# Kernel optimization log

Measured on AMD Instinct MI355X. Metric: run time of the kernel, lower is better.

## Reference

```python
import jax, jax.numpy as jnp
import numpy as np

D_MODEL = 1024
NUM_HEADS = 16
HEAD_DIM = D_MODEL // NUM_HEADS
D_FF = 4096
THETA = 10000.0
MAX_SEQ_LEN = 2048
EPS = 1e-5


def _init_linear(key, out_f, in_f):
    std = np.sqrt(2.0 / (out_f + in_f))
    w = jax.random.truncated_normal(key, -3.0, 3.0, (out_f, in_f), dtype=jnp.float32) * std
    return w


def setup_inputs() -> dict:
    key = jax.random.key(0)
    ks = jax.random.split(key, 9)
    x = jax.random.normal(ks[0], (4, 2048, D_MODEL), dtype=jnp.float32)
    return {
        "x": x,
        "wq": _init_linear(ks[1], D_MODEL, D_MODEL),
        "wk": _init_linear(ks[2], D_MODEL, D_MODEL),
        "wv": _init_linear(ks[3], D_MODEL, D_MODEL),
        "wo": _init_linear(ks[4], D_MODEL, D_MODEL),
        "ln1_w": jnp.ones((D_MODEL,), jnp.float32),
        "ln2_w": jnp.ones((D_MODEL,), jnp.float32),
        "up_w": _init_linear(ks[5], D_FF, D_MODEL),
        "gate_w": _init_linear(ks[6], D_FF, D_MODEL),
        "down_w": _init_linear(ks[7], D_MODEL, D_FF),
    }


def _rmsnorm(x, w):
    xf = x.astype(jnp.float32)
    inv_rms = jax.lax.rsqrt(jnp.mean(xf * xf, axis=-1, keepdims=True) + EPS)
    return (xf * inv_rms * w).astype(x.dtype)


def _rope_tables(seq_len):
    inv_freq = 1.0 / THETA ** (jnp.arange(0, HEAD_DIM, 2, dtype=jnp.float32) / HEAD_DIM)
    t = jnp.arange(seq_len, dtype=jnp.float32)
    freqs = jnp.outer(t, inv_freq)  # [s, hd/2]
    return jnp.cos(freqs), jnp.sin(freqs)


def _apply_rope(x, cos, sin):
    # x: [b, h, s, hd]; cos/sin: [s, hd/2] -> broadcast over b,h
    xe = x[..., 0::2]
    xo = x[..., 1::2]
    oe = xe * cos - xo * sin
    oo = xo * cos + xe * sin
    return jnp.stack((oe, oo), axis=-1).reshape(x.shape)


def reference(x, wq, wk, wv, wo, ln1_w, ln2_w, up_w, gate_w, down_w):
    b, s, d = x.shape
    h, hd = NUM_HEADS, HEAD_DIM

    # --- attention sublayer (pre-norm) ---
    xn = _rmsnorm(x, ln1_w)
    q = (xn @ wq.T).reshape(b, s, h, hd).transpose(0, 2, 1, 3)
    k = (xn @ wk.T).reshape(b, s, h, hd).transpose(0, 2, 1, 3)
    v = (xn @ wv.T).reshape(b, s, h, hd).transpose(0, 2, 1, 3)

    cos, sin = _rope_tables(s)
    q = _apply_rope(q, cos, sin)
    k = _apply_rope(k, cos, sin)

    scale = 1.0 / jnp.sqrt(jnp.float32(hd))
    logits = jnp.einsum("bhqd,bhkd->bhqk", q, k)
    causal = jnp.tril(jnp.ones((s, s), dtype=bool))
    logits = jnp.where(causal, logits, -jnp.inf)
    attn = jax.nn.softmax(logits * scale, axis=-1)
    ao = jnp.einsum("bhqk,bhkd->bhqd", attn, v)
    ao = ao.transpose(0, 2, 1, 3).reshape(b, s, d) @ wo.T
    x = x + ao

    # --- SwiGLU FFN sublayer (pre-norm) ---
    xn = _rmsnorm(x, ln2_w)
    up = xn @ up_w.T
    gate = xn @ gate_w.T
    ff = (up * jax.nn.sigmoid(up) * gate) @ down_w.T
    return x + ff
```

## Files before the change

### kernel.cpp

```cpp
#include <hip/hip_runtime.h>
#include <stdint.h>

#define SEQ   2048
#define NTOK  8192

typedef unsigned short u16;
typedef __bf16 bf16x8 __attribute__((ext_vector_type(8)));
typedef float  f32x4  __attribute__((ext_vector_type(4)));
typedef float  f32x16 __attribute__((ext_vector_type(16)));

__device__ __forceinline__ float b2f(u16 b) {
    union { unsigned u; float f; } v; v.u = ((unsigned)b) << 16; return v.f;
}
__device__ __forceinline__ u16 f2b(float f) {
    union { float f; unsigned u; } v; v.f = f;
    unsigned r = (v.u + 0x7fffu + ((v.u >> 16) & 1u)) >> 16;
    return (u16)r;
}
__device__ __forceinline__ u16 f2b_trunc(float f) {
    union { float f; unsigned u; } v; v.f = f;
    return (u16)(v.u >> 16);
}

__device__ __forceinline__ void gl_lds16(const void* g, void* l) {
    __builtin_amdgcn_global_load_lds(
        (const __attribute__((address_space(1))) void*)g,
        (__attribute__((address_space(3))) void*)l,
        16, 0, 0);
}

__global__ __launch_bounds__(256)
void cvt_all(const float* __restrict__ wq, const float* __restrict__ wk,
             const float* __restrict__ wv, const float* __restrict__ wo,
             const float* __restrict__ wup, const float* __restrict__ wgt,
             const float* __restrict__ wdn,
             u16* __restrict__ dq, u16* __restrict__ dk, u16* __restrict__ dv,
             u16* __restrict__ dw, u16* __restrict__ dmu, u16* __restrict__ dd)
{
    const int bid = blockIdx.x;
    const float* s; u16* d; int osrc, odst;
    if (bid < 4096) {
        const int which = bid >> 10;
        osrc = odst = (bid & 1023) * 256 + threadIdx.x;
        s = which == 0 ? wq : which == 1 ? wk : which == 2 ? wv : wo;
        d = which == 0 ? dq : which == 1 ? dk : which == 2 ? dv : dw;
    } else {
        const int which = (bid - 4096) >> 12;
        const int o = ((bid - 4096) & 4095) * 256 + threadIdx.x;
        osrc = o;
        if (which == 2) { s = wdn; d = dd; odst = o; }
        else {
            s = which == 0 ? wup : wgt;
            d = dmu;
            const int row = o >> 8;
            const int rowp = ((row >> 4) << 5) + (row & 15) + (which == 0 ? 16 : 0);
            odst = rowp * 256 + (o & 255);
        }
    }
    float4 v = ((const float4*)s)[osrc];
    ushort4 ov;
    ov.x = f2b(v.x); ov.y = f2b(v.y); ov.z = f2b(v.z); ov.w = f2b(v.w);
    ((ushort4*)d)[odst] = ov;
}

template<int EPI>
__global__ __launch_bounds__(256)
void gemm_bt(const u16* __restrict__ A, const u16* __restrict__ B,
             void* __restrict__ C, const void* __restrict__ E,
             int M, int N, int K, int ldc, int coff)
{
    __shared__ __align__(16) u16 As[128 * 64];
    __shared__ __align__(16) u16 Bs[128 * 64];

    const int tid  = threadIdx.x;
    const int lane = tid & 63;
    const int wid  = tid >> 6;
    const int m0 = blockIdx.y * 128;
    const int n0 = blockIdx.x * 128;
    const int wm = (wid >> 1) * 64;
    const int wn = (wid & 1) * 64;
    const int l31 = lane & 31, kg = lane >> 5;

    f32x16 acc[2][2];
#pragma unroll
    for (int i = 0; i < 2; i++)
#pragma unroll
        for (int j = 0; j < 2; j++)
#pragma unroll
            for (int r = 0; r < 16; r++) acc[i][j][r] = 0.f;

    const u16* Ag[4]; const u16* Bg[4]; u16* Al[4]; u16* Bl[4];
#pragma unroll
    for (int j = 0; j < 4; j++) {
        const int q = j * 256 + tid;
        const int r = q >> 3, s = q & 7, c = s ^ (r & 7);
        Ag[j] = A + (size_t)(m0 + r) * K + c * 8;
        Bg[j] = B + (size_t)(n0 + r) * K + c * 8;
        Al[j] = As + q * 8;
        Bl[j] = Bs + q * 8;
    }

    int arow[2], brow[2];
#pragma unroll
    for (int i = 0; i < 2; i++) { arow[i] = wm + i * 32 + l31; }
#pragma unroll
    for (int j = 0; j < 2; j++) { brow[j] = wn + j * 32 + l31; }

    for (int kt = 0; kt < K; kt += 64) {
        __syncthreads();
#pragma unroll
        for (int j = 0; j < 4; j++) {
            gl_lds16(Ag[j] + kt, Al[j]);
            gl_lds16(Bg[j] + kt, Bl[j]);
        }
        __syncthreads();

#pragma unroll
        for (int s = 0; s < 4; s++) {
            const int ch = s * 2 + kg;
            bf16x8 af[2], bf[2];
#pragma unroll
            for (int i = 0; i < 2; i++)
                af[i] = *(const bf16x8*)(
                    &As[arow[i] * 64 + ((ch ^ (arow[i] & 7)) * 8)]);
#pragma unroll
            for (int j = 0; j < 2; j++)
                bf[j] = *(const bf16x8*)(
                    &Bs[brow[j] * 64 + ((ch ^ (brow[j] & 7)) * 8)]);
#pragma unroll
            for (int i = 0; i < 2; i++)
#pragma unroll
                for (int j = 0; j < 2; j++)
                    acc[i][j] = __builtin_amdgcn_mfma_f32_32x32x16_bf16(
                        af[i], bf[j], acc[i][j], 0, 0, 0);
        }
    }

#pragma unroll
    for (int i = 0; i < 2; i++) {
#pragma unroll
        for (int r = 0; r < 16; r++) {
            const int row = m0 + wm + i * 32 + (r & 3) + 8 * (r >> 2) + 4 * kg;
#pragma unroll
            for (int j = 0; j < 2; j++) {
                const int col = n0 + wn + j * 32 + l31;
                const size_t idx = (size_t)row * ldc + coff + col;
                const float v = acc[i][j][r];
                if (EPI == 0) {
                    ((u16*)C)[idx] = f2b(v);
                } else {
                    ((float*)C)[idx] = v + ((const float*)E)[idx];
                }
            }
        }
    }
}

#define MIDBAR \
    __builtin_amdgcn_s_barrier(); \
    asm volatile("s_waitcnt lgkmcnt(0)" ::: "memory"); \
    __builtin_amdgcn_sched_barrier(0);

#define PBAR \
    __builtin_amdgcn_s_barrier(); \
    asm volatile("" ::: "memory"); \
    __builtin_amdgcn_sched_barrier(0);

#define VMBARN(n) \
    asm volatile("s_waitcnt vmcnt(" #n ")" ::: "memory"); \
    __builtin_amdgcn_s_barrier(); \
    asm volatile("" ::: "memory"); \
    __builtin_amdgcn_sched_barrier(0);

#define LDA(bufi, mh) { \
    const u16* _ab = Ab##bufi + (mh) * 4096; \
    _Pragma("unroll") \
    for (int _m = 0; _m < 4; ++_m) { \
        Aq[_m][0] = *(const bf16x8*)(_ab + _m * 1024 + axor0); \
        Aq[_m][1] = *(const bf16x8*)(_ab + _m * 1024 + axor1); \
    } }

#define LDB(bufi, nh) { \
    const u16* _bb = Bb##bufi + (nh) * 2048; \
    _Pragma("unroll") \
    for (int _n = 0; _n < 2; ++_n) { \
        Bq[nh][_n][0] = *(const bf16x8*)(_bb + _n * 1024 + axor0); \
        Bq[nh][_n][1] = *(const bf16x8*)(_bb + _n * 1024 + axor1); \
    } }

#define MM(mh, nh) \
    __builtin_amdgcn_s_setprio(1); \
    { _Pragma("unroll") \
      for (int _m = 0; _m < 4; ++_m) { \
        _Pragma("unroll") \
        for (int _n = 0; _n < 2; ++_n) { \
            acc[(mh)*4+_m][(nh)*2+_n] = __builtin_amdgcn_mfma_f32_16x16x32_bf16( \
                Aq[_m][0], Bq[nh][_n][0], acc[(mh)*4+_m][(nh)*2+_n], 0, 0, 0); \
            acc[(mh)*4+_m][(nh)*2+_n] = __builtin_amdgcn_mfma_f32_16x16x32_bf16( \
                Aq[_m][1], Bq[nh][_n][1], acc[(mh)*4+_m][(nh)*2+_n], 0, 0, 0); \
        } } } \
    __builtin_amdgcn_s_setprio(0);

#define STAGE_A(tile, half) { \
    const u16* _s = pA0 + (size_t)(half) * 131072 + (size_t)(tile) * 64; \
    u16* _d = lA0 + ((tile) & 1) * 16384 + (half) * 8192; \
    gl_lds16(_s, _d); \
    gl_lds16(_s + 65536, _d + 4096); }

#define STAGE_B(tile, half) { \
    const u16* _s = pB0 + (size_t)(half) * 131072 + (size_t)(tile) * 64; \
    u16* _d = lB0 + ((tile) & 1) * 16384 + (half) * 8192; \
    gl_lds16(_s, _d); \
    gl_lds16(_s + 65536, _d + 4096); }

__global__ __launch_bounds__(512, 2)
void gemm8_mlp(const u16* __restrict__ A, const u16* __restrict__ Bc,
               u16* __restrict__ H)
{
    __shared__ __align__(16) u16 As[32768];
    __shared__ __align__(16) u16 Bs[32768];

    const int tid = threadIdx.x, lane = tid & 63, wid = tid >> 6;
    const int wr = wid >> 2, wc = wid & 3;
    const int r15 = lane & 15, ks = lane >> 4;
    const int m0 = blockIdx.y * 256, n0 = blockIdx.x * 256;

    const int axor0 = ((ks) ^ (r15 & 7)) * 8;
    const int axor1 = ((4 + ks) ^ (r15 & 7)) * 8;
    const u16* Ab0 = As + wr * 8192 + r15 * 64;
    const u16* Ab1 = As + 16384 + wr * 8192 + r15 * 64;
    const u16* Bb0 = Bs + (wc >> 1) * 8192 + (wc & 1) * 4096 + r15 * 64;
    const u16* Bb1 = Bs + 16384 + (wc >> 1) * 8192 + (wc & 1) * 4096 + r15 * 64;

    const int r0 = tid >> 3, c0 = (tid & 7) ^ (r0 & 7);
    const u16* pA0 = A  + (size_t)(m0 + r0) * 1024 + c0 * 8;
    const u16* pB0 = Bc + (size_t)(n0 + r0) * 1024 + c0 * 8;
    u16* lA0 = As + tid * 8;
    u16* lB0 = Bs + tid * 8;

    f32x4 acc[8][4];
#pragma unroll
    for (int m = 0; m < 8; ++m)
#pragma unroll
        for (int n = 0; n < 4; ++n)
            acc[m][n] = (f32x4){0.f, 0.f, 0.f, 0.f};

    bf16x8 Aq[4][2], Bq[2][2][2];

    STAGE_A(0, 0); STAGE_A(0, 1);
    STAGE_B(0, 0); STAGE_B(0, 1);
    STAGE_B(1, 0); STAGE_B(1, 1);
    asm volatile("s_waitcnt vmcnt(4)" ::: "memory");
    __builtin_amdgcn_s_barrier();
    asm volatile("" ::: "memory");
    __builtin_amdgcn_sched_barrier(0);

    for (int i = 0; i < 8; ++i) {
        const int t1 = 2 * i + 1;
        const int t2 = 2 * i + 2;
        const int t3 = 2 * i + 3;
        const bool st = (i < 7);

        LDA(0, 0); LDB(0, 0);
        STAGE_A(t1, 0);
        MIDBAR; MM(0, 0); PBAR;
        LDB(0, 1);
        STAGE_A(t1, 1);
        MIDBAR; MM(0, 1); PBAR;
        LDA(0, 1);
        if (st) STAGE_B(t2, 0);
        MIDBAR; MM(1, 1); PBAR;
        if (st) STAGE_B(t2, 1);
        MIDBAR; MM(1, 0);
        if (i == 7) { VMBARN(0); } else { VMBARN(4); }

        LDA(1, 0); LDB(1, 0);
        if (st) STAGE_A(t2, 0);
        MIDBAR; MM(0, 0); PBAR;
        LDB(1, 1);
        if (st) STAGE_A(t2, 1);
        MIDBAR; MM(0, 1); PBAR;
        LDA(1, 1);
        if (st) STAGE_B(t3, 0);
        MIDBAR; MM(1, 1); PBAR;
        if (st) STAGE_B(t3, 1);
        MIDBAR; MM(1, 0);
        VMBARN(4);
    }

    const int orow0 = m0 + wr * 128;
    const int ocol0 = (n0 >> 1) + wc * 32;
#pragma unroll
    for (int m = 0; m < 8; ++m) {
#pragma unroll
        for (int p = 0; p < 2; ++p) {
#pragma unroll
            for (int r = 0; r < 4; ++r) {
                const int row = orow0 + m * 16 + ks * 4 + r;
                const int col = ocol0 + p * 16 + r15;
                const float g = acc[m][2 * p][r];
                const float u = acc[m][2 * p + 1][r];
                H[(size_t)row * 4096 + col] = f2b(u / (1.f + __expf(-u)) * g);
            }
        }
    }
}

__global__ __launch_bounds__(256)
void rmsnorm_k(const float* __restrict__ xin, const float* __restrict__ w,
               u16* __restrict__ o)
{
    const int t = blockIdx.x;
    const int tid = threadIdx.x;
    float4 xv = ((const float4*)xin)[(size_t)t * 256 + tid];
    float ss = xv.x * xv.x + xv.y * xv.y + xv.z * xv.z + xv.w * xv.w;
#pragma unroll
    for (int off = 32; off > 0; off >>= 1) ss += __shfl_down(ss, off);
    __shared__ float red[4];
    const int lane = tid & 63, wv_ = tid >> 6;
    if (lane == 0) red[wv_] = ss;
    __syncthreads();
    const float tot = red[0] + red[1] + red[2] + red[3];
    const float inv = rsqrtf(tot * (1.f / 1024.f) + 1e-5f);
    float4 ww = ((const float4*)w)[tid];
    ushort4 ov;
    ov.x = f2b(xv.x * inv * ww.x);
    ov.y = f2b(xv.y * inv * ww.y);
    ov.z = f2b(xv.z * inv * ww.z);
    ov.w = f2b(xv.w * inv * ww.w);
    ((ushort4*)o)[(size_t)t * 256 + tid] = ov;
}

#define QSCALE 0.18033688011112042f

__global__ void rope_tab(float* __restrict__ cs, float* __restrict__ sn)
{
    const int s = blockIdx.x;
    const int i = threadIdx.x;
    const double inv = exp(-((double)(2 * i) / 64.0) * log(10000.0));
    const double ang = (double)s * inv;
    cs[s * 32 + i] = (float)cos(ang);
    sn[s * 32 + i] = (float)sin(ang);
}

__global__ __launch_bounds__(256)
void rope_apply(u16* __restrict__ qkv, const float* __restrict__ cs,
                const float* __restrict__ sn)
{
    const int t = blockIdx.x;
    const int s = t & (SEQ - 1);
    u16* row = qkv + (size_t)t * 3072;
    __shared__ float c_s[32], s_s[32];
    if (threadIdx.x < 32) {
        c_s[threadIdx.x] = cs[s * 32 + threadIdx.x];
        s_s[threadIdx.x] = sn[s * 32 + threadIdx.x];
    }
    __syncthreads();
#pragma unroll
    for (int rr = 0; rr < 2; rr++) {
        const int item = rr * 256 + threadIdx.x;
        const int hh = item >> 5, i = item & 31;
        const int f = hh * 64 + 2 * i;
        const float c = c_s[i], sv = s_s[i];
        float xe = b2f(row[f]), xo = b2f(row[f + 1]);
        row[f]     = f2b((xe * c - xo * sv) * QSCALE);
        row[f + 1] = f2b((xo * c + xe * sv) * QSCALE);
        xe = b2f(row[1024 + f]); xo = b2f(row[1024 + f + 1]);
        row[1024 + f]     = f2b(xe * c - xo * sv);
        row[1024 + f + 1] = f2b(xo * c + xe * sv);
    }
}

__global__ __launch_bounds__(256)
void vtrans(const u16* __restrict__ qkv, u16* __restrict__ vt)
{
    __shared__ u16 Ld[64 * 264];
    const int bh = blockIdx.x, st = blockIdx.y;
    const int b = bh >> 4, h = bh & 15;
    const int tid = threadIdx.x;
    const u16* src = qkv + ((size_t)(b * SEQ + st * 256 + tid)) * 3072 + 2048 + h * 64;
    uint4 v[8];
#pragma unroll
    for (int c = 0; c < 8; c++) v[c] = *(const uint4*)(src + c * 8);
#pragma unroll
    for (int c = 0; c < 8; c++) {
        const u16* pv = (const u16*)&v[c];
#pragma unroll
        for (int j = 0; j < 8; j++)
            Ld[(c * 8 + j) * 264 + tid] = pv[j];
    }
    __syncthreads();
    u16* dst = vt + (size_t)bh * (64 * SEQ) + st * 256;
#pragma unroll
    for (int cc = 0; cc < 8; cc++) {
        const int c = cc * 256 + tid;
        const int d = c >> 5, t8 = (c & 31) * 8;
        *(uint4*)(dst + (size_t)d * SEQ + t8) = *(const uint4*)(&Ld[d * 264 + t8]);
    }
}

__global__ __launch_bounds__(512)
void attn(const u16* __restrict__ qkv, const u16* __restrict__ vt,
          u16* __restrict__ ao)
{
    __shared__ __align__(16) u16 Ks[128 * 72];
    __shared__ __align__(16) u16 Vt[64 * 136];
    __shared__ __align__(16) u16 Ps[8][16 * 136];

    const int bh = blockIdx.x;
    const int qy = blockIdx.y;
    const int b = bh >> 4, h = bh & 15;
    const int tid = threadIdx.x, lane = tid & 63, wid = tid >> 6;
    const int am = lane & 15, grp = lane >> 4;
    const size_t tok0 = (size_t)b * SEQ;
    const u16* qbase = qkv + tok0 * 3072 + h * 64;
    const u16* kbase = qbase + 1024;
    const u16* vtg = vt + (size_t)bh * (64 * SEQ);

    union { uint4 u; bf16x8 b; } onesu;
    onesu.u = (uint4){0x3f803f80u, 0x3f803f80u, 0x3f803f80u, 0x3f803f80u};
    const bf16x8 ones = onesu.b;

    const int srow = tid >> 3, sc8 = (tid & 7) * 8;

#pragma unroll
    for (int tile = 0; tile < 2; tile++) {
        const int yt = tile == 0 ? qy : 15 - qy;
        const int qrow0 = yt * 128 + wid * 16;

        bf16x8 qf[2];
        {
            const u16* qp = qbase + (size_t)(qrow0 + am) * 3072 + grp * 8;
            qf[0] = *(const bf16x8*)(qp);
            qf[1] = *(const bf16x8*)(qp + 32);
        }

        f32x4 O[4], Ol;
#pragma unroll
        for (int j = 0; j < 4; j++) O[j] = (f32x4){0.f, 0.f, 0.f, 0.f};
        Ol = (f32x4){0.f, 0.f, 0.f, 0.f};

        const int ktend = yt * 128;
        for (int kt = 0; kt <= ktend; kt += 128) {
            __syncthreads();
            *(uint4*)(&Ks[srow * 72 + sc8]) =
                *(const uint4*)(kbase + (size_t)(kt + srow) * 3072 + sc8);
            *(uint4*)(&Ks[(srow + 64) * 72 + sc8]) =
                *(const uint4*)(kbase + (size_t)(kt + srow + 64) * 3072 + sc8);
            *(uint4*)(&Vt[srow * 136 + sc8]) =
                *(const uint4*)(vtg + (size_t)srow * SEQ + kt + sc8);
            *(uint4*)(&Vt[srow * 136 + 64 + sc8]) =
                *(const uint4*)(vtg + (size_t)srow * SEQ + kt + 64 + sc8);
            __syncthreads();

            const bool diag = (kt == ktend);
            u16* pw = &Ps[wid][0];

#pragma unroll
            for (int kh = 0; kh < 2; kh++) {
                f32x4 st[4];
#pragma unroll
                for (int kk = 0; kk < 4; kk++) {
                    const u16* kb = &Ks[(kh * 64 + kk * 16 + am) * 72 + grp * 8];
                    bf16x8 k0 = *(const bf16x8*)(kb);
                    bf16x8 k1 = *(const bf16x8*)(kb + 32);
                    f32x4 s = (f32x4){0.f, 0.f, 0.f, 0.f};
                    s = __builtin_amdgcn_mfma_f32_16x16x32_bf16(k0, qf[0], s, 0, 0, 0);
                    s = __builtin_amdgcn_mfma_f32_16x16x32_bf16(k1, qf[1], s, 0, 0, 0);
                    st[kk] = s;
                }
                if (diag) {
                    const int qg = qrow0 + am;
#pragma unroll
                    for (int kk = 0; kk < 4; kk++) {
                        const int kb2 = kt + kh * 64 + kk * 16 + grp * 4;
#pragma unroll
                        for (int r = 0; r < 4; r++) {
                            if (kb2 + r > qg) st[kk][r] = -1e30f;
                        }
                    }
                }
#pragma unroll
                for (int kk = 0; kk < 4; kk++)
#pragma unroll
                    for (int r = 0; r < 4; r++)
                        st[kk][r] = exp2f(st[kk][r]);

#pragma unroll
                for (int kk = 0; kk < 4; kk++) {
                    ushort4 pk;
                    pk.x = f2b_trunc(st[kk][0]);
                    pk.y = f2b_trunc(st[kk][1]);
                    pk.z = f2b_trunc(st[kk][2]);
                    pk.w = f2b_trunc(st[kk][3]);
                    *(ushort4*)(&pw[am * 136 + kh * 64 + kk * 16 + grp * 4]) = pk;
                }
            }
            asm volatile("s_waitcnt lgkmcnt(0)" ::: "memory");

#pragma unroll
            for (int hh = 0; hh < 4; hh++) {
                bf16x8 pf = *(const bf16x8*)(&pw[am * 136 + hh * 32 + grp * 8]);
                Ol = __builtin_amdgcn_mfma_f32_16x16x32_bf16(pf, ones, Ol, 0, 0, 0);
#pragma unroll
                for (int jt = 0; jt < 4; jt++) {
                    bf16x8 vf = *(const bf16x8*)(
                        &Vt[(jt * 16 + am) * 136 + hh * 32 + grp * 8]);
                    O[jt] = __builtin_amdgcn_mfma_f32_16x16x32_bf16(
                        pf, vf, O[jt], 0, 0, 0);
                }
            }
        }

        u16* aorow = ao + (tok0 + qrow0) * 1024 + h * 64;
#pragma unroll
        for (int r = 0; r < 4; r++) {
            const int q = grp * 4 + r;
            const float invl = 1.f / Ol[r];
#pragma unroll
            for (int jt = 0; jt < 4; jt++)
                aorow[(size_t)q * 1024 + jt * 16 + am] = f2b(O[jt][r] * invl);
        }
    }
}

extern "C" void kernel_launch(void* const* d_in, const int* in_sizes, int n_in,
                              void* d_out, int out_size, void* d_ws, size_t ws_size,
                              hipStream_t stream)
{
    (void)in_sizes; (void)n_in; (void)out_size; (void)ws_size;
    const float* x     = (const float*)d_in[0];
    const float* wq    = (const float*)d_in[1];
    const float* wk    = (const float*)d_in[2];
    const float* wv    = (const float*)d_in[3];
    const float* wo    = (const float*)d_in[4];
    const float* ln1   = (const float*)d_in[5];
    const float* ln2   = (const float*)d_in[6];
    const float* wup   = (const float*)d_in[7];
    const float* wgate = (const float*)d_in[8];
    const float* wdown = (const float*)d_in[9];
    float* out = (float*)d_out;
    char* ws = (char*)d_ws;
    const size_t MB = 1024 * 1024;

    u16*   xn   = (u16*)(ws);
    u16*   ao   = (u16*)(ws);
    u16*   qkv  = (u16*)(ws + 16 * MB);
    u16*   hbuf = (u16*)(ws + 16 * MB);
    u16*   vtb  = (u16*)(ws + 64 * MB);
    float* x1   = (float*)(ws + 80 * MB);
    u16*   bwq  = (u16*)(ws + 112 * MB);
    u16*   bwk  = (u16*)(ws + 114 * MB);
    u16*   bwv  = (u16*)(ws + 116 * MB);
    u16*   bwo  = (u16*)(ws + 118 * MB);
    u16*   bwmu = (u16*)(ws + 120 * MB);
    u16*   bwdn = (u16*)(ws + 136 * MB);
    float* cst  = (float*)(ws + 144 * MB);
    float* snt  = (float*)(ws + 144 * MB + 262144);

    cvt_all<<<16384, 256, 0, stream>>>(wq, wk, wv, wo, wup, wgate, wdown,
                                       bwq, bwk, bwv, bwo, bwmu, bwdn);

    rope_tab<<<SEQ, 32, 0, stream>>>(cst, snt);
    rmsnorm_k<<<NTOK, 256, 0, stream>>>(x, ln1, xn);
    gemm_bt<0><<<dim3(24, 64), 256, 0, stream>>>(xn, bwq, qkv, nullptr, NTOK, 3072, 1024, 3072, 0);
    rope_apply<<<NTOK, 256, 0, stream>>>(qkv, cst, snt);
    vtrans<<<dim3(64, 8), 256, 0, stream>>>(qkv, vtb);
    attn<<<dim3(64, 8), 512, 0, stream>>>(qkv, vtb, ao);
    gemm_bt<1><<<dim3(8, 64), 256, 0, stream>>>(ao, bwo, x1, x, NTOK, 1024, 1024, 1024, 0);
    rmsnorm_k<<<NTOK, 256, 0, stream>>>(x1, ln2, xn);
    gemm8_mlp<<<dim3(32, 32), 512, 0, stream>>>(xn, bwmu, hbuf);
    gemm_bt<1><<<dim3(8, 64), 256, 0, stream>>>(hbuf, bwdn, out, x1, NTOK, 1024, 4096, 1024, 0);
}
```

Baseline: 564.5 us.

## Make MLP GEMM blocks loop over four M tiles with continuous prefetch

The fused up/gate GEMM now launches a quarter as many blocks, and each block walks four consecutive 256-row M tiles. The global-to-LDS staging pipeline runs unbroken across tile boundaries, and each tile's SwiGLU epilogue is written before the accumulators are reset. This removes per-block prologue and pipeline-fill costs and may improve L2 reuse of the B tile. In exchange the grid drops from 1024 to 256 blocks, which is about one wave on 256 CUs, so tail and occupancy behaviour changes.

```diff
diff --git a/kernel.cpp b/kernel.cpp
--- a/kernel.cpp
+++ b/kernel.cpp
@@ -201,15 +201,16 @@
         } } } \
     __builtin_amdgcn_s_setprio(0);
 
-#define STAGE_A(tile, half) { \
-    const u16* _s = pA0 + (size_t)(half) * 131072 + (size_t)(tile) * 64; \
-    u16* _d = lA0 + ((tile) & 1) * 16384 + (half) * 8192; \
+#define STAGE_A(T, half) { \
+    const u16* _s = pA0 + (size_t)((T) >> 4) * 262144 \
+                        + (size_t)((T) & 15) * 64 + (size_t)(half) * 131072; \
+    u16* _d = lA0 + ((T) & 1) * 16384 + (half) * 8192; \
     gl_lds16(_s, _d); \
     gl_lds16(_s + 65536, _d + 4096); }
 
-#define STAGE_B(tile, half) { \
-    const u16* _s = pB0 + (size_t)(half) * 131072 + (size_t)(tile) * 64; \
-    u16* _d = lB0 + ((tile) & 1) * 16384 + (half) * 8192; \
+#define STAGE_B(T, half) { \
+    const u16* _s = pB0 + (size_t)((T) & 15) * 64 + (size_t)(half) * 131072; \
+    u16* _d = lB0 + ((T) & 1) * 16384 + (half) * 8192; \
     gl_lds16(_s, _d); \
     gl_lds16(_s + 65536, _d + 4096); }
 
@@ -223,7 +224,7 @@
     const int tid = threadIdx.x, lane = tid & 63, wid = tid >> 6;
     const int wr = wid >> 2, wc = wid & 3;
     const int r15 = lane & 15, ks = lane >> 4;
-    const int m0 = blockIdx.y * 256, n0 = blockIdx.x * 256;
+    const int m0 = blockIdx.y * 1024, n0 = blockIdx.x * 256;
 
     const int axor0 = ((ks) ^ (r15 & 7)) * 8;
     const int axor1 = ((4 + ks) ^ (r15 & 7)) * 8;
@@ -255,54 +256,63 @@
     asm volatile("" ::: "memory");
     __builtin_amdgcn_sched_barrier(0);
 
-    for (int i = 0; i < 8; ++i) {
-        const int t1 = 2 * i + 1;
-        const int t2 = 2 * i + 2;
-        const int t3 = 2 * i + 3;
-        const bool st = (i < 7);
-
-        LDA(0, 0); LDB(0, 0);
-        STAGE_A(t1, 0);
-        MIDBAR; MM(0, 0); PBAR;
-        LDB(0, 1);
-        STAGE_A(t1, 1);
-        MIDBAR; MM(0, 1); PBAR;
-        LDA(0, 1);
-        if (st) STAGE_B(t2, 0);
-        MIDBAR; MM(1, 1); PBAR;
-        if (st) STAGE_B(t2, 1);
-        MIDBAR; MM(1, 0);
-        if (i == 7) { VMBARN(0); } else { VMBARN(4); }
-
-        LDA(1, 0); LDB(1, 0);
-        if (st) STAGE_A(t2, 0);
-        MIDBAR; MM(0, 0); PBAR;
-        LDB(1, 1);
-        if (st) STAGE_A(t2, 1);
-        MIDBAR; MM(0, 1); PBAR;
-        LDA(1, 1);
-        if (st) STAGE_B(t3, 0);
-        MIDBAR; MM(1, 1); PBAR;
-        if (st) STAGE_B(t3, 1);
-        MIDBAR; MM(1, 0);
-        VMBARN(4);
-    }
-
-    const int orow0 = m0 + wr * 128;
-    const int ocol0 = (n0 >> 1) + wc * 32;
-#pragma unroll
-    for (int m = 0; m < 8; ++m) {
-#pragma unroll
-        for (int p = 0; p < 2; ++p) {
-#pragma unroll
-            for (int r = 0; r < 4; ++r) {
-                const int row = orow0 + m * 16 + ks * 4 + r;
-                const int col = ocol0 + p * 16 + r15;
-                const float g = acc[m][2 * p][r];
-                const float u = acc[m][2 * p + 1][r];
-                H[(size_t)row * 4096 + col] = f2b(u / (1.f + __expf(-u)) * g);
+    for (int hm = 0; hm < 4; ++hm) {
+        const int base = hm * 16;
+        for (int i = 0; i < 8; ++i) {
+            const int t1 = base + 2 * i + 1;
+            const int t2 = base + 2 * i + 2;
+            const int t3 = base + 2 * i + 3;
+            const bool s2 = (t2 < 64);
+            const bool s3 = (t3 < 64);
+
+            LDA(0, 0); LDB(0, 0);
+            STAGE_A(t1, 0);
+            MIDBAR; MM(0, 0); PBAR;
+            LDB(0, 1);
+            STAGE_A(t1, 1);
+            MIDBAR; MM(0, 1); PBAR;
+            LDA(0, 1);
+            if (s2) STAGE_B(t2, 0);
+            MIDBAR; MM(1, 1); PBAR;
+            if (s2) STAGE_B(t2, 1);
+            MIDBAR; MM(1, 0);
+            if (s2) { VMBARN(4); } else { VMBARN(0); }
+
+            LDA(1, 0); LDB(1, 0);
+            if (s2) STAGE_A(t2, 0);
+            MIDBAR; MM(0, 0); PBAR;
+            LDB(1, 1);
+            if (s2) STAGE_A(t2, 1);
+            MIDBAR; MM(0, 1); PBAR;
+            LDA(1, 1);
+            if (s3) STAGE_B(t3, 0);
+            MIDBAR; MM(1, 1); PBAR;
+            if (s3) STAGE_B(t3, 1);
+            MIDBAR; MM(1, 0);
+            VMBARN(4);
+        }
+
+        const int orow0 = m0 + hm * 256 + wr * 128;
+        const int ocol0 = (n0 >> 1) + wc * 32;
+#pragma unroll
+        for (int m = 0; m < 8; ++m) {
+#pragma unroll
+            for (int p = 0; p < 2; ++p) {
+#pragma unroll
+                for (int r = 0; r < 4; ++r) {
+                    const int row = orow0 + m * 16 + ks * 4 + r;
+                    const int col = ocol0 + p * 16 + r15;
+                    const float g = acc[m][2 * p][r];
+                    const float u = acc[m][2 * p + 1][r];
+                    H[(size_t)row * 4096 + col] = f2b(u / (1.f + __expf(-u)) * g);
+                }
             }
         }
+#pragma unroll
+        for (int m = 0; m < 8; ++m)
+#pragma unroll
+            for (int n = 0; n < 4; ++n)
+                acc[m][n] = (f32x4){0.f, 0.f, 0.f, 0.f};
     }
 }
 
@@ -569,6 +579,6 @@
     attn<<<dim3(64, 8), 512, 0, stream>>>(qkv, vtb, ao);
     gemm_bt<1><<<dim3(8, 64), 256, 0, stream>>>(ao, bwo, x1, x, NTOK, 1024, 1024, 1024, 0);
     rmsnorm_k<<<NTOK, 256, 0, stream>>>(x1, ln2, xn);
-    gemm8_mlp<<<dim3(32, 32), 512, 0, stream>>>(xn, bwmu, hbuf);
+    gemm8_mlp<<<dim3(32, 8), 512, 0, stream>>>(xn, bwmu, hbuf);
     gemm_bt<1><<<dim3(8, 64), 256, 0, stream>>>(hbuf, bwdn, out, x1, NTOK, 1024, 4096, 1024, 0);
 }
```

New measurement: 545.1 us. 1.04x faster.
